# Kernel optimization log

Hardware: AMD Instinct MI355X
Metric: run time of the kernel (lower is better)

## Reference

```python
import jax, jax.numpy as jnp
import numpy as np
from jax import lax

DN = ('NHWC', 'HWIO', 'NHWC')

def _conv(a, w):
    return lax.conv_general_dilated(a, w, (1, 1), 'SAME', dimension_numbers=DN)

def _hard_sigmoid(z):
    return jnp.clip(0.2 * z + 0.5, 0.0, 1.0)


def setup_inputs() -> dict:
    key = jax.random.key(0)
    ks = jax.random.split(key, 4)
    B, T, H, W, C, F, K = 2, 16, 64, 64, 64, 64, 3
    x = jax.random.normal(ks[0], (B, T, H, W, C), dtype=jnp.float32)
    Wx = jax.random.normal(ks[1], (K, K, C, 4 * F), dtype=jnp.float32) * (2.0 / (K * K * C)) ** 0.5
    Wh = jax.random.normal(ks[2], (K, K, F, 4 * F), dtype=jnp.float32) * (2.0 / (K * K * F)) ** 0.5
    b = jax.random.normal(ks[3], (4 * F,), dtype=jnp.float32) * 0.01
    gamma = jnp.ones((F,), dtype=jnp.float32)
    beta = jnp.zeros((F,), dtype=jnp.float32)
    moving_mean = jnp.zeros((F,), dtype=jnp.float32)
    moving_var = jnp.ones((F,), dtype=jnp.float32)
    return {"x": x, "Wx": Wx, "Wh": Wh, "b": b, "gamma": gamma,
            "beta": beta, "moving_mean": moving_mean, "moving_var": moving_var}


def reference(x, Wx, Wh, b, gamma, beta, moving_mean, moving_var):
    B, T, H, W, C = x.shape
    F = Wh.shape[2]
    # Precompute the input-to-gate convolutions for all timesteps in one big conv.
    xg = _conv(x.reshape(B * T, H, W, C), Wx) + b          # (B*T, H, W, 4F)
    xg = xg.reshape(B, T, H, W, 4 * F).transpose(1, 0, 2, 3, 4)  # (T, B, H, W, 4F)

    h0 = jnp.zeros((B, H, W, F), dtype=x.dtype)
    c0 = jnp.zeros((B, H, W, F), dtype=x.dtype)

    def step(carry, xt):
        h, c = carry
        z = xt + _conv(h, Wh)                               # (B, H, W, 4F)
        zi, zf, zg, zo = jnp.split(z, 4, axis=-1)           # Keras gate order: i, f, c, o
        i = _hard_sigmoid(zi)
        f = _hard_sigmoid(zf)
        g = jnp.tanh(zg)
        o = _hard_sigmoid(zo)
        c_new = f * c + i * g
        h_new = o * jnp.tanh(c_new)
        return (h_new, c_new), h_new

    _, hs = lax.scan(step, (h0, c0), xg)                    # (T, B, H, W, F)
    out = hs.transpose(1, 0, 2, 3, 4)                       # (B, T, H, W, F)

    # BatchNormalization in inference mode (training=False), eps=1e-3 (Keras default)
    eps = 1e-3
    inv = gamma * lax.rsqrt(moving_var + eps)
    out = out * inv + (beta - moving_mean * inv)
    return out
```

## Files before the change

kernel.cpp:

```cpp
#include <hip/hip_runtime.h>
#include <cstddef>

typedef __attribute__((ext_vector_type(8))) _Float16 half8;
typedef __attribute__((ext_vector_type(4))) float f32x4;
typedef __attribute__((ext_vector_type(4))) unsigned short us4;

#define TT 16
#define APAD 72
#define A_TILE (3*34*APAD)
#define XA_TILE (3*66*APAD)
#define CHUNK  8192
#define NBUF   6
#define PFDIST 5

__device__ __forceinline__ unsigned short f2h(float f) {
    return __builtin_bit_cast(unsigned short, (_Float16)f);
}
__device__ __forceinline__ float h2f(unsigned short u) {
    return (float)__builtin_bit_cast(_Float16, u);
}
__device__ __forceinline__ float hsig(float z) {
    return fminf(fmaxf(0.2f * z + 0.5f, 0.f), 1.f);
}

typedef __attribute__((address_space(3))) unsigned int lds_uint;
typedef const __attribute__((address_space(1))) unsigned int glb_uint;
__device__ __forceinline__ void async16(const void* g, void* l) {
    __builtin_amdgcn_global_load_lds((glb_uint*)g, (lds_uint*)l, 16, 0, 0);
}

#define WAITVM(N) { asm volatile("s_waitcnt vmcnt(" #N ")" ::: "memory"); \
                    __builtin_amdgcn_sched_barrier(0); }

__global__ __launch_bounds__(256) void prep_kernel(
    const float* __restrict__ Wx, const float* __restrict__ Wh,
    const float* __restrict__ gamma, const float* __restrict__ beta,
    const float* __restrict__ mean, const float* __restrict__ var,
    unsigned short* __restrict__ Wc, float* __restrict__ bn)
{
    if (blockIdx.x == 1152) {
        if (threadIdx.x < 64) {
            const int c = threadIdx.x;
            const float inv = gamma[c] * rsqrtf(var[c] + 1e-3f);
            bn[c] = inv;
            bn[64 + c] = beta[c] - mean[c] * inv;
        }
        return;
    }
    const int i = blockIdx.x * 256 + threadIdx.x;
    const int j  = i & 7;
    const int n  = (i >> 3) & 255;
    const int kg = (i >> 11) & 3;
    const int s  = i >> 13;
    const int sub = s % 18;
    const float* W = (s >= 18) ? Wh : Wx;
    const int k5 = sub * 32 + kg * 8 + j;
    const int c = k5 & 63, q = k5 >> 6;
    const int kx = q % 3, ky = q / 3;
    Wc[i] = f2h(W[(size_t)((ky * 3 + kx) * 64 + c) * 256 + n]);
}

template<int C0, int CLAST, int AOFF>
__device__ __forceinline__ void conv_pass18(
    const unsigned short* __restrict__ Wc,
    const int soff0, const int soff1,
    unsigned short* lds0, unsigned short* lds1,
    const unsigned short* abase,
    const unsigned short* bbase,
    f32x4 acc[2][2])
{
    #pragma unroll
    for (int sub = 0; sub < 18; ++sub) {
        const int ci = C0 + sub;
        if (ci + PFDIST <= CLAST) {
            const int sc = ci + PFDIST;
            const unsigned short* gsc = Wc + (size_t)sc * CHUNK;
            const int bsel = (sc % NBUF) * CHUNK;
            async16(gsc + soff0, lds0 + bsel);
            async16(gsc + soff1, lds1 + bsel);
        }
        const int rem = CLAST - ci;
        if (rem >= PFDIST) WAITVM(10)
        else if (rem == 4) WAITVM(8)
        else if (rem == 3) WAITVM(6)
        else if (rem == 2) WAITVM(4)
        else if (rem == 1) WAITVM(2)
        else               WAITVM(0)

        const int ky = sub / 6, kx = (sub / 2) % 3, cb = sub & 1;
        const int aimm = (ky * 34 + kx) * APAD + cb * 32;
        const unsigned short* bbuf = bbase + (ci % NBUF) * CHUNK;

        const half8 b0 = *(const half8*)(bbuf);
        const half8 b1 = *(const half8*)(bbuf + 128);
        const unsigned short* at = abase + AOFF + aimm;
        const half8 a0 = *(const half8*)(at);
        const half8 a1 = *(const half8*)(at + 16 * APAD);
        acc[0][0] = __builtin_amdgcn_mfma_f32_16x16x32_f16(a0, b0, acc[0][0], 0, 0, 0);
        acc[0][1] = __builtin_amdgcn_mfma_f32_16x16x32_f16(a0, b1, acc[0][1], 0, 0, 0);
        acc[1][0] = __builtin_amdgcn_mfma_f32_16x16x32_f16(a1, b0, acc[1][0], 0, 0, 0);
        acc[1][1] = __builtin_amdgcn_mfma_f32_16x16x32_f16(a1, b1, acc[1][1], 0, 0, 0);
    }
}

__global__ __launch_bounds__(512) void xconv_kernel(
    const float* __restrict__ x,
    const unsigned short* __restrict__ Wc,
    const float* __restrict__ bias,
    unsigned short* __restrict__ xg)
{
    const int bid0 = blockIdx.x;
    const int bid = (bid0 & 7) * 256 + (bid0 >> 3);
    const int y = bid & 63;
    const int t = (bid >> 6) & 15;
    const int n = bid >> 10;
    const int tid = threadIdx.x, lane = tid & 63, w = tid >> 6;

    __shared__ __align__(16) unsigned short smem[XA_TILE + NBUF * CHUNK];

    const int soff0 = ((lane >> 5)    ) * 2048 + (w * 32 + (lane & 31)) * 8;
    const int soff1 = ((lane >> 5) + 2) * 2048 + (w * 32 + (lane & 31)) * 8;
    unsigned short* lds0 = smem + XA_TILE + w * 1024 + (lane     ) * 8;
    unsigned short* lds1 = smem + XA_TILE + w * 1024 + (64 + lane) * 8;
    #pragma unroll
    for (int sc = 0; sc < PFDIST; ++sc) {
        const unsigned short* gsc = Wc + (size_t)sc * CHUNK;
        async16(gsc + soff0, lds0 + sc * CHUNK);
        async16(gsc + soff1, lds1 + sc * CHUNK);
    }

    const float* __restrict__ xt = x + (size_t)(n * TT + t) * 4096 * 64;
    for (int idx = tid; idx < 3 * 66 * 8; idx += 512) {
        const int cg  = idx & 7;
        const int col = (idx >> 3) % 66;
        const int r   = (idx >> 3) / 66;
        const int gy = y + r - 1;
        const int gx = col - 1;
        const bool ok = ((unsigned)gy < 64u) && ((unsigned)gx < 64u);
        float4 v0 = make_float4(0.f, 0.f, 0.f, 0.f), v1 = v0;
        if (ok) {
            const float* p = xt + (size_t)(gy * 64 + gx) * 64 + cg * 8;
            v0 = *(const float4*)p;
            v1 = *(const float4*)(p + 4);
        }
        us4 h0, h1;
        h0.x = f2h(v0.x); h0.y = f2h(v0.y); h0.z = f2h(v0.z); h0.w = f2h(v0.w);
        h1.x = f2h(v1.x); h1.y = f2h(v1.y); h1.z = f2h(v1.z); h1.w = f2h(v1.w);
        const int ebase = (r * 66 + col) * APAD + cg * 8;
        *(us4*)&smem[ebase]     = h0;
        *(us4*)&smem[ebase + 4] = h1;
    }
    __syncthreads();

    const int p0 = lane & 15, g = lane >> 4;
    const unsigned short* abase = smem + p0 * APAD + g * 8;
    const unsigned short* bbase = smem + XA_TILE + w * 1024 + (g * 32 + p0) * 8;

    f32x4 acc[4][2] = {};
    #pragma unroll
    for (int sub = 0; sub < 18; ++sub) {
        if (sub + PFDIST < 18) {
            const int sc = sub + PFDIST;
            const unsigned short* gsc = Wc + (size_t)sc * CHUNK;
            const int bsel = (sc % NBUF) * CHUNK;
            async16(gsc + soff0, lds0 + bsel);
            async16(gsc + soff1, lds1 + bsel);
        }
        const int rem = 17 - sub;
        if (rem >= PFDIST) WAITVM(10)
        else if (rem == 4) WAITVM(8)
        else if (rem == 3) WAITVM(6)
        else if (rem == 2) WAITVM(4)
        else if (rem == 1) WAITVM(2)
        else               WAITVM(0)

        const int ky = sub / 6, kx = (sub / 2) % 3, cb = sub & 1;
        const unsigned short* bbuf = bbase + (sub % NBUF) * CHUNK;
        const half8 b0 = *(const half8*)(bbuf);
        const half8 b1 = *(const half8*)(bbuf + 128);
        #pragma unroll
        for (int mf = 0; mf < 4; ++mf) {
            const half8 a = *(const half8*)(abase + (ky * 66 + kx + mf * 16) * APAD + cb * 32);
            acc[mf][0] = __builtin_amdgcn_mfma_f32_16x16x32_f16(a, b0, acc[mf][0], 0, 0, 0);
            acc[mf][1] = __builtin_amdgcn_mfma_f32_16x16x32_f16(a, b1, acc[mf][1], 0, 0, 0);
        }
    }

    const float bv0 = bias[w * 32 + p0];
    const float bv1 = bias[w * 32 + 16 + p0];
    const size_t vibase = ((((size_t)(n * TT + t) * 64 + y) * 2) * 8 + w) * 64 + lane;
    #pragma unroll
    for (int xh2 = 0; xh2 < 2; ++xh2) {
        unsigned short os[16];
        #pragma unroll
        for (int mfc = 0; mfc < 2; ++mfc)
            #pragma unroll
            for (int nf = 0; nf < 2; ++nf)
                #pragma unroll
                for (int j = 0; j < 4; ++j)
                    os[mfc * 8 + nf * 4 + j] =
                        f2h(acc[xh2 * 2 + mfc][nf][j] + (nf ? bv1 : bv0));
        unsigned short* dst = xg + (vibase + (size_t)xh2 * 512) * 16;
        *(uint4*)dst       = *(uint4*)&os[0];
        *(uint4*)(dst + 8) = *(uint4*)&os[8];
    }
}

template<int FUSED>
__global__ __launch_bounds__(512) void convstep_kernel(
    const float* __restrict__ x,
    const unsigned short* __restrict__ hb,
    const unsigned short* __restrict__ Wc,
    const float* __restrict__ bias,
    const unsigned short* __restrict__ xg,
    float* __restrict__ cbuf,
    unsigned short* __restrict__ ho,
    const float* __restrict__ bn,
    float* __restrict__ out,
    const int t)
{
    const int bid0 = blockIdx.x;
    const int bid = (bid0 & 7) * 32 + (bid0 >> 3);
    const int xh = bid & 1;
    const int y  = (bid >> 1) & 63;
    const int n  = bid >> 7;
    const int tid = threadIdx.x;
    const int lane = tid & 63;
    const int w = tid >> 6;
    const int p0 = lane & 15;
    const int g  = lane >> 4;

    constexpr int NTILE = FUSED ? 2 : 1;
    constexpr int BOFF  = NTILE * A_TILE;
    __shared__ __align__(16) unsigned short smem[NTILE * A_TILE + NBUF * CHUNK];

    unsigned short xs[16];
    if (!FUSED) {
        const size_t vi = ((((size_t)(n * TT + t) * 64 + y) * 2 + xh) * 8 + w) * 64 + lane;
        const uint4* xp = (const uint4*)(xg + vi * 16);
        *(uint4*)&xs[0] = xp[0];
        *(uint4*)&xs[8] = xp[1];
    }

    constexpr int C0 = FUSED ? 0 : 18;
    const int soff0 = ((lane >> 5)    ) * 2048 + (w * 32 + (lane & 31)) * 8;
    const int soff1 = ((lane >> 5) + 2) * 2048 + (w * 32 + (lane & 31)) * 8;
    unsigned short* lds0 = smem + BOFF + w * 1024 + (lane     ) * 8;
    unsigned short* lds1 = smem + BOFF + w * 1024 + (64 + lane) * 8;
    #pragma unroll
    for (int sc = C0; sc < C0 + PFDIST; ++sc) {
        const unsigned short* gsc = Wc + (size_t)sc * CHUNK;
        async16(gsc + soff0, lds0 + (sc % NBUF) * CHUNK);
        async16(gsc + soff1, lds1 + (sc % NBUF) * CHUNK);
    }

    const float* __restrict__ xt = x + (size_t)(n * TT + t) * 4096 * 64;
    const size_t hbase = (size_t)n * 4096 * 64;
    for (int idx = tid; idx < NTILE * 3 * 34 * 8; idx += 512) {
        const int cg  = idx & 7;
        const int col = (idx >> 3) % 34;
        const int i3  = (idx >> 3) / 34;
        const int r   = i3 % 3;
        const int src = i3 / 3;
        const int gy = y + r - 1;
        const int gx = xh * 32 + col - 1;
        const bool ok = ((unsigned)gy < 64u) && ((unsigned)gx < 64u);
        const int ebase = (r * 34 + col) * APAD + cg * 8;
        if (FUSED && src == 0) {
            float4 v0 = make_float4(0.f, 0.f, 0.f, 0.f), v1 = v0;
            if (ok) {
                const float* p = xt + (size_t)(gy * 64 + gx) * 64 + cg * 8;
                v0 = *(const float4*)p;
                v1 = *(const float4*)(p + 4);
            }
            us4 h0, h1;
            h0.x = f2h(v0.x); h0.y = f2h(v0.y); h0.z = f2h(v0.z); h0.w = f2h(v0.w);
            h1.x = f2h(v1.x); h1.y = f2h(v1.y); h1.z = f2h(v1.z); h1.w = f2h(v1.w);
            *(us4*)&smem[ebase]     = h0;
            *(us4*)&smem[ebase + 4] = h1;
        } else {
            uint4 v = make_uint4(0u, 0u, 0u, 0u);
            if (ok) v = *(const uint4*)(hb + hbase + (size_t)(gy * 64 + gx) * 64 + cg * 8);
            *(uint4*)&smem[(FUSED ? A_TILE : 0) + ebase] = v;
        }
    }
    __syncthreads();

    const unsigned short* abase = smem + p0 * APAD + g * 8;
    const unsigned short* bbase = smem + BOFF + w * 1024 + (g * 32 + p0) * 8;

    f32x4 acc[2][2] = {};
    if (FUSED) {
        conv_pass18<0, 35, 0>(Wc, soff0, soff1, lds0, lds1, abase, bbase, acc);
        conv_pass18<18, 35, A_TILE>(Wc, soff0, soff1, lds0, lds1, abase, bbase, acc);
    } else {
        conv_pass18<18, 35, 0>(Wc, soff0, soff1, lds0, lds1, abase, bbase, acc);
    }

    __syncthreads();
    float* gbuf = (float*)smem;
    const int gate = w >> 1;
    const int chalf = (w & 1) * 32;

    float bv[2];
    bv[0] = bias[w * 32 + p0];
    bv[1] = bias[w * 32 + 16 + p0];

    #pragma unroll
    for (int mf = 0; mf < 2; ++mf)
        #pragma unroll
        for (int nf = 0; nf < 2; ++nf)
            #pragma unroll
            for (int j = 0; j < 4; ++j) {
                float v = acc[mf][nf][j] + (FUSED ? bv[nf] : h2f(xs[mf * 8 + nf * 4 + j]));
                v = (gate == 2) ? tanhf(v) : hsig(v);
                const int px = mf * 16 + g * 4 + j;
                gbuf[(gate * 32 + px) * 68 + chalf + nf * 16 + p0] = v;
            }
    __syncthreads();

    const int p  = tid >> 4;
    const int c4 = (tid & 15) * 4;
    const float4 iv = *(const float4*)&gbuf[(0 * 32 + p) * 68 + c4];
    const float4 fv = *(const float4*)&gbuf[(1 * 32 + p) * 68 + c4];
    const float4 gv = *(const float4*)&gbuf[(2 * 32 + p) * 68 + c4];
    const float4 ov = *(const float4*)&gbuf[(3 * 32 + p) * 68 + c4];
    const size_t gpix = (size_t)((n * 64 + y) * 64 + xh * 32 + p);
    const size_t sb = gpix * 64 + c4;
    const float4 cold = *(const float4*)&cbuf[sb];
    const float4 scv  = *(const float4*)&bn[c4];
    const float4 shv  = *(const float4*)&bn[64 + c4];

    const float ivv[4] = {iv.x, iv.y, iv.z, iv.w};
    const float fvv[4] = {fv.x, fv.y, fv.z, fv.w};
    const float gvv[4] = {gv.x, gv.y, gv.z, gv.w};
    const float ovv[4] = {ov.x, ov.y, ov.z, ov.w};
    const float cov[4] = {cold.x, cold.y, cold.z, cold.w};
    const float scc[4] = {scv.x, scv.y, scv.z, scv.w};
    const float shh[4] = {shv.x, shv.y, shv.z, shv.w};

    float cnew[4], obuf[4];
    us4 hh;
    unsigned short* hhp = (unsigned short*)&hh;
    #pragma unroll
    for (int j = 0; j < 4; ++j) {
        const float cn = fvv[j] * cov[j] + ivv[j] * gvv[j];
        const float hn = ovv[j] * tanhf(cn);
        cnew[j] = cn;
        hhp[j] = f2h(hn);
        obuf[j] = hn * scc[j] + shh[j];
    }
    *(float4*)&cbuf[sb] = *(float4*)&cnew[0];
    *(us4*)&ho[sb]      = hh;
    const size_t ob = ((size_t)((n * TT + t) * 4096 + y * 64 + xh * 32 + p)) * 64 + c4;
    *(float4*)&out[ob] = *(float4*)&obuf[0];
}

extern "C" void kernel_launch(void* const* d_in, const int* in_sizes, int n_in,
                              void* d_out, int out_size, void* d_ws, size_t ws_size,
                              hipStream_t stream) {
    const float* x     = (const float*)d_in[0];
    const float* Wx    = (const float*)d_in[1];
    const float* Wh    = (const float*)d_in[2];
    const float* b     = (const float*)d_in[3];
    const float* gamma = (const float*)d_in[4];
    const float* beta  = (const float*)d_in[5];
    const float* mean  = (const float*)d_in[6];
    const float* var   = (const float*)d_in[7];
    float* out = (float*)d_out;
    char* ws = (char*)d_ws;

    unsigned short* Wc   = (unsigned short*)(ws);
    float*          bn   = (float*)(ws + 589824);
    unsigned short* hA   = (unsigned short*)(ws + 590336);
    float*          cbuf = (float*)(ws + 1638912);
    unsigned short* hB   = (unsigned short*)(ws + 3736064);
    unsigned short* xg   = (unsigned short*)(ws + 4784640);
    const size_t NEED = 4784640ull + 67108864ull;

    hipMemsetAsync(ws + 590336, 0, 3145728, stream);
    prep_kernel<<<1153, 256, 0, stream>>>(Wx, Wh, gamma, beta, mean, var, Wc, bn);

    if (ws_size >= NEED) {
        xconv_kernel<<<2048, 512, 0, stream>>>(x, Wc, b, xg);
        for (int t = 0; t < TT; ++t) {
            const bool even = (t & 1) == 0;
            convstep_kernel<0><<<256, 512, 0, stream>>>(
                x, even ? hA : hB, Wc, b, xg, cbuf, even ? hB : hA, bn, out, t);
        }
    } else {
        for (int t = 0; t < TT; ++t) {
            const bool even = (t & 1) == 0;
            convstep_kernel<1><<<256, 512, 0, stream>>>(
                x, even ? hA : hB, Wc, b, xg, cbuf, even ? hB : hA, bn, out, t);
        }
    }
}
```

Before: 206.5 us.

## Load conv weights directly into registers and process two rows per xconv block

Weight chunks are no longer staged through LDS with async global-to-LDS copies and explicit vmcnt waits. Each lane now prefetches its B fragments straight into a ring of registers with ordinary global loads. The input-conv kernel also computes two output rows per block (half as many blocks), so each weight fragment feeds twice as many MFMAs, and its LDS footprint shrinks. In exchange, register pressure rises considerably (6x2 half8 prefetch slots plus 16 accumulators), which may cut occupancy. Without the explicit waits, the compiler now decides when to wait on these loads.

```diff
diff --git a/kernel.cpp b/kernel.cpp
--- a/kernel.cpp
+++ b/kernel.cpp
@@ -8,10 +8,9 @@
 #define TT 16
 #define APAD 72
 #define A_TILE (3*34*APAD)
-#define XA_TILE (3*66*APAD)
 #define CHUNK  8192
-#define NBUF   6
-#define PFDIST 5
+#define NB     6
+#define PF     5
 
 __device__ __forceinline__ unsigned short f2h(float f) {
     return __builtin_bit_cast(unsigned short, (_Float16)f);
@@ -22,15 +21,6 @@
 __device__ __forceinline__ float hsig(float z) {
     return fminf(fmaxf(0.2f * z + 0.5f, 0.f), 1.f);
 }
-
-typedef __attribute__((address_space(3))) unsigned int lds_uint;
-typedef const __attribute__((address_space(1))) unsigned int glb_uint;
-__device__ __forceinline__ void async16(const void* g, void* l) {
-    __builtin_amdgcn_global_load_lds((glb_uint*)g, (lds_uint*)l, 16, 0, 0);
-}
-
-#define WAITVM(N) { asm volatile("s_waitcnt vmcnt(" #N ")" ::: "memory"); \
-                    __builtin_amdgcn_sched_barrier(0); }
 
 __global__ __launch_bounds__(256) void prep_kernel(
     const float* __restrict__ Wx, const float* __restrict__ Wh,
@@ -60,40 +50,28 @@
     Wc[i] = f2h(W[(size_t)((ky * 3 + kx) * 64 + c) * 256 + n]);
 }
 
+#define BLOAD(slot, ci) {                                                     \
+    const unsigned short* _p = Wc + (size_t)(ci) * CHUNK + boff;              \
+    bp[slot][0] = *(const half8*)_p;                                          \
+    bp[slot][1] = *(const half8*)(_p + 128);                                  \
+}
+
 template<int C0, int CLAST, int AOFF>
 __device__ __forceinline__ void conv_pass18(
-    const unsigned short* __restrict__ Wc,
-    const int soff0, const int soff1,
-    unsigned short* lds0, unsigned short* lds1,
+    const unsigned short* __restrict__ Wc, const int boff,
+    half8 (&bp)[NB][2],
     const unsigned short* abase,
-    const unsigned short* bbase,
     f32x4 acc[2][2])
 {
     #pragma unroll
     for (int sub = 0; sub < 18; ++sub) {
         const int ci = C0 + sub;
-        if (ci + PFDIST <= CLAST) {
-            const int sc = ci + PFDIST;
-            const unsigned short* gsc = Wc + (size_t)sc * CHUNK;
-            const int bsel = (sc % NBUF) * CHUNK;
-            async16(gsc + soff0, lds0 + bsel);
-            async16(gsc + soff1, lds1 + bsel);
-        }
-        const int rem = CLAST - ci;
-        if (rem >= PFDIST) WAITVM(10)
-        else if (rem == 4) WAITVM(8)
-        else if (rem == 3) WAITVM(6)
-        else if (rem == 2) WAITVM(4)
-        else if (rem == 1) WAITVM(2)
-        else               WAITVM(0)
+        if (ci + PF <= CLAST) BLOAD((ci + PF) % NB, ci + PF)
 
         const int ky = sub / 6, kx = (sub / 2) % 3, cb = sub & 1;
-        const int aimm = (ky * 34 + kx) * APAD + cb * 32;
-        const unsigned short* bbuf = bbase + (ci % NBUF) * CHUNK;
-
-        const half8 b0 = *(const half8*)(bbuf);
-        const half8 b1 = *(const half8*)(bbuf + 128);
-        const unsigned short* at = abase + AOFF + aimm;
+        const half8 b0 = bp[ci % NB][0];
+        const half8 b1 = bp[ci % NB][1];
+        const unsigned short* at = abase + AOFF + (ky * 34 + kx) * APAD + cb * 32;
         const half8 a0 = *(const half8*)(at);
         const half8 a1 = *(const half8*)(at + 16 * APAD);
         acc[0][0] = __builtin_amdgcn_mfma_f32_16x16x32_f16(a0, b0, acc[0][0], 0, 0, 0);
@@ -110,31 +88,27 @@
     unsigned short* __restrict__ xg)
 {
     const int bid0 = blockIdx.x;
-    const int bid = (bid0 & 7) * 256 + (bid0 >> 3);
-    const int y = bid & 63;
-    const int t = (bid >> 6) & 15;
-    const int n = bid >> 10;
+    const int bid = (bid0 & 7) * 128 + (bid0 >> 3);
+    const int y0 = (bid & 31) * 2;
+    const int t  = (bid >> 5) & 15;
+    const int n  = bid >> 9;
     const int tid = threadIdx.x, lane = tid & 63, w = tid >> 6;
-
-    __shared__ __align__(16) unsigned short smem[XA_TILE + NBUF * CHUNK];
-
-    const int soff0 = ((lane >> 5)    ) * 2048 + (w * 32 + (lane & 31)) * 8;
-    const int soff1 = ((lane >> 5) + 2) * 2048 + (w * 32 + (lane & 31)) * 8;
-    unsigned short* lds0 = smem + XA_TILE + w * 1024 + (lane     ) * 8;
-    unsigned short* lds1 = smem + XA_TILE + w * 1024 + (64 + lane) * 8;
-    #pragma unroll
-    for (int sc = 0; sc < PFDIST; ++sc) {
-        const unsigned short* gsc = Wc + (size_t)sc * CHUNK;
-        async16(gsc + soff0, lds0 + sc * CHUNK);
-        async16(gsc + soff1, lds1 + sc * CHUNK);
-    }
+    const int p0 = lane & 15, g = lane >> 4;
+
+    __shared__ __align__(16) unsigned short smem[4 * 66 * APAD];
+
+    const int boff = g * 2048 + (w * 32 + p0) * 8;
+
+    half8 bp[NB][2];
+    #pragma unroll
+    for (int sc = 0; sc < PF; ++sc) BLOAD(sc, sc)
 
     const float* __restrict__ xt = x + (size_t)(n * TT + t) * 4096 * 64;
-    for (int idx = tid; idx < 3 * 66 * 8; idx += 512) {
+    for (int idx = tid; idx < 4 * 66 * 8; idx += 512) {
         const int cg  = idx & 7;
         const int col = (idx >> 3) % 66;
         const int r   = (idx >> 3) / 66;
-        const int gy = y + r - 1;
+        const int gy = y0 + r - 1;
         const int gx = col - 1;
         const bool ok = ((unsigned)gy < 64u) && ((unsigned)gx < 64u);
         float4 v0 = make_float4(0.f, 0.f, 0.f, 0.f), v1 = v0;
@@ -152,35 +126,21 @@
     }
     __syncthreads();
 
-    const int p0 = lane & 15, g = lane >> 4;
     const unsigned short* abase = smem + p0 * APAD + g * 8;
-    const unsigned short* bbase = smem + XA_TILE + w * 1024 + (g * 32 + p0) * 8;
-
-    f32x4 acc[4][2] = {};
+
+    f32x4 acc[8][2] = {};
     #pragma unroll
     for (int sub = 0; sub < 18; ++sub) {
-        if (sub + PFDIST < 18) {
-            const int sc = sub + PFDIST;
-            const unsigned short* gsc = Wc + (size_t)sc * CHUNK;
-            const int bsel = (sc % NBUF) * CHUNK;
-            async16(gsc + soff0, lds0 + bsel);
-            async16(gsc + soff1, lds1 + bsel);
-        }
-        const int rem = 17 - sub;
-        if (rem >= PFDIST) WAITVM(10)
-        else if (rem == 4) WAITVM(8)
-        else if (rem == 3) WAITVM(6)
-        else if (rem == 2) WAITVM(4)
-        else if (rem == 1) WAITVM(2)
-        else               WAITVM(0)
+        if (sub + PF < 18) BLOAD((sub + PF) % NB, sub + PF)
 
         const int ky = sub / 6, kx = (sub / 2) % 3, cb = sub & 1;
-        const unsigned short* bbuf = bbase + (sub % NBUF) * CHUNK;
-        const half8 b0 = *(const half8*)(bbuf);
-        const half8 b1 = *(const half8*)(bbuf + 128);
+        const half8 b0 = bp[sub % NB][0];
+        const half8 b1 = bp[sub % NB][1];
         #pragma unroll
-        for (int mf = 0; mf < 4; ++mf) {
-            const half8 a = *(const half8*)(abase + (ky * 66 + kx + mf * 16) * APAD + cb * 32);
+        for (int mf = 0; mf < 8; ++mf) {
+            const int r = mf >> 2, cq = mf & 3;
+            const half8 a = *(const half8*)(abase
+                + ((r + ky) * 66 + cq * 16 + kx) * APAD + cb * 32);
             acc[mf][0] = __builtin_amdgcn_mfma_f32_16x16x32_f16(a, b0, acc[mf][0], 0, 0, 0);
             acc[mf][1] = __builtin_amdgcn_mfma_f32_16x16x32_f16(a, b1, acc[mf][1], 0, 0, 0);
         }
@@ -188,22 +148,24 @@
 
     const float bv0 = bias[w * 32 + p0];
     const float bv1 = bias[w * 32 + 16 + p0];
-    const size_t vibase = ((((size_t)(n * TT + t) * 64 + y) * 2) * 8 + w) * 64 + lane;
-    #pragma unroll
-    for (int xh2 = 0; xh2 < 2; ++xh2) {
-        unsigned short os[16];
+    #pragma unroll
+    for (int r = 0; r < 2; ++r)
         #pragma unroll
-        for (int mfc = 0; mfc < 2; ++mfc)
+        for (int xh2 = 0; xh2 < 2; ++xh2) {
+            unsigned short os[16];
             #pragma unroll
-            for (int nf = 0; nf < 2; ++nf)
+            for (int mfc = 0; mfc < 2; ++mfc)
                 #pragma unroll
-                for (int j = 0; j < 4; ++j)
-                    os[mfc * 8 + nf * 4 + j] =
-                        f2h(acc[xh2 * 2 + mfc][nf][j] + (nf ? bv1 : bv0));
-        unsigned short* dst = xg + (vibase + (size_t)xh2 * 512) * 16;
-        *(uint4*)dst       = *(uint4*)&os[0];
-        *(uint4*)(dst + 8) = *(uint4*)&os[8];
-    }
+                for (int nf = 0; nf < 2; ++nf)
+                    #pragma unroll
+                    for (int j = 0; j < 4; ++j)
+                        os[mfc * 8 + nf * 4 + j] =
+                            f2h(acc[r * 4 + xh2 * 2 + mfc][nf][j] + (nf ? bv1 : bv0));
+            const size_t vi = ((((size_t)(n * TT + t) * 64 + (y0 + r)) * 2 + xh2) * 8 + w) * 64 + lane;
+            unsigned short* dst = xg + vi * 16;
+            *(uint4*)dst       = *(uint4*)&os[0];
+            *(uint4*)(dst + 8) = *(uint4*)&os[8];
+        }
 }
 
 template<int FUSED>
@@ -230,9 +192,10 @@
     const int p0 = lane & 15;
     const int g  = lane >> 4;
 
-    constexpr int NTILE = FUSED ? 2 : 1;
-    constexpr int BOFF  = NTILE * A_TILE;
-    __shared__ __align__(16) unsigned short smem[NTILE * A_TILE + NBUF * CHUNK];
+    constexpr int SMEM_SHORTS = FUSED ? (2 * A_TILE) : 17408;
+    __shared__ __align__(16) unsigned short smem[SMEM_SHORTS];
+
+    const int boff = g * 2048 + (w * 32 + p0) * 8;
 
     unsigned short xs[16];
     if (!FUSED) {
@@ -243,17 +206,11 @@
     }
 
     constexpr int C0 = FUSED ? 0 : 18;
-    const int soff0 = ((lane >> 5)    ) * 2048 + (w * 32 + (lane & 31)) * 8;
-    const int soff1 = ((lane >> 5) + 2) * 2048 + (w * 32 + (lane & 31)) * 8;
-    unsigned short* lds0 = smem + BOFF + w * 1024 + (lane     ) * 8;
-    unsigned short* lds1 = smem + BOFF + w * 1024 + (64 + lane) * 8;
-    #pragma unroll
-    for (int sc = C0; sc < C0 + PFDIST; ++sc) {
-        const unsigned short* gsc = Wc + (size_t)sc * CHUNK;
-        async16(gsc + soff0, lds0 + (sc % NBUF) * CHUNK);
-        async16(gsc + soff1, lds1 + (sc % NBUF) * CHUNK);
-    }
-
+    half8 bp[NB][2];
+    #pragma unroll
+    for (int sc = 0; sc < PF; ++sc) BLOAD((C0 + sc) % NB, C0 + sc)
+
+    constexpr int NTILE = FUSED ? 2 : 1;
     const float* __restrict__ xt = x + (size_t)(n * TT + t) * 4096 * 64;
     const size_t hbase = (size_t)n * 4096 * 64;
     for (int idx = tid; idx < NTILE * 3 * 34 * 8; idx += 512) {
@@ -287,14 +244,13 @@
     __syncthreads();
 
     const unsigned short* abase = smem + p0 * APAD + g * 8;
-    const unsigned short* bbase = smem + BOFF + w * 1024 + (g * 32 + p0) * 8;
 
     f32x4 acc[2][2] = {};
     if (FUSED) {
-        conv_pass18<0, 35, 0>(Wc, soff0, soff1, lds0, lds1, abase, bbase, acc);
-        conv_pass18<18, 35, A_TILE>(Wc, soff0, soff1, lds0, lds1, abase, bbase, acc);
+        conv_pass18<0, 35, 0>(Wc, boff, bp, abase, acc);
+        conv_pass18<18, 35, A_TILE>(Wc, boff, bp, abase, acc);
     } else {
-        conv_pass18<18, 35, 0>(Wc, soff0, soff1, lds0, lds1, abase, bbase, acc);
+        conv_pass18<18, 35, 0>(Wc, boff, bp, abase, acc);
     }
 
     __syncthreads();
@@ -382,7 +338,7 @@
     prep_kernel<<<1153, 256, 0, stream>>>(Wx, Wh, gamma, beta, mean, var, Wc, bn);
 
     if (ws_size >= NEED) {
-        xconv_kernel<<<2048, 512, 0, stream>>>(x, Wc, b, xg);
+        xconv_kernel<<<1024, 512, 0, stream>>>(x, Wc, b, xg);
         for (int t = 0; t < TT; ++t) {
             const bool even = (t & 1) == 0;
             convstep_kernel<0><<<256, 512, 0, stream>>>(
```

New measurement: 203.1 us. Within noise of the previous version (-1.6%).
